# Performance work log

Hardware: AMD Instinct MI355X
Metric: run time of the kernel (lower is better)

## Reference

```python
import jax, jax.numpy as jnp
import numpy as np

# model dims
V, D, C, H, NL, E, EH = 32000, 256, 2, 8, 2, 8, 1024
B, S = 16, 512
DH = D // H
N = B * S


def _pos_encoding(length, d):
    pos = jnp.arange(length)[:, None].astype(jnp.float32)
    div = jnp.exp(jnp.arange(0, d, 2).astype(jnp.float32) * (-np.log(10000.0) / d))
    pe = jnp.zeros((length, d), dtype=jnp.float32)
    pe = pe.at[:, 0::2].set(jnp.sin(pos * div))
    pe = pe.at[:, 1::2].set(jnp.cos(pos * div))
    return pe


def _ln(x, g, b, eps=1e-5):
    mu = x.mean(-1, keepdims=True)
    var = ((x - mu) ** 2).mean(-1, keepdims=True)
    return (x - mu) / jnp.sqrt(var + eps) * g + b


def setup_inputs():
    key = jax.random.key(0)
    ks = jax.random.split(key, 12)
    n = lambda k, shape, s=0.02: (jax.random.normal(k, shape) * s).astype(jnp.float32)
    return dict(
        x=jax.random.randint(ks[0], (B, S), 0, V),
        emb=n(ks[1], (V, D), 0.1),
        in_proj_w=n(ks[2], (NL, 3 * D, D)),
        in_proj_b=jnp.zeros((NL, 3 * D), jnp.float32),
        out_proj_w=n(ks[3], (NL, D, D)),
        out_proj_b=jnp.zeros((NL, D), jnp.float32),
        ln1_g=jnp.ones((NL, D), jnp.float32), ln1_b=jnp.zeros((NL, D), jnp.float32),
        ln2_g=jnp.ones((NL, D), jnp.float32), ln2_b=jnp.zeros((NL, D), jnp.float32),
        gate_w=n(ks[4], (NL, E, D)), gate_b=jnp.zeros((NL, E), jnp.float32),
        w1=n(ks[5], (NL, E, EH, D)), b1=jnp.zeros((NL, E, EH), jnp.float32),
        w2=n(ks[6], (NL, E, D, EH)), b2=jnp.zeros((NL, E, D), jnp.float32),
        fc1_w=n(ks[7], (128, D), 0.1), fc1_b=jnp.zeros((128,), jnp.float32),
        fc2_w=n(ks[8], (C, 128), 0.1), fc2_b=jnp.zeros((C,), jnp.float32),
    )


def reference(x, emb, in_proj_w, in_proj_b, out_proj_w, out_proj_b,
              ln1_g, ln1_b, ln2_g, ln2_b, gate_w, gate_b,
              w1, b1, w2, b2, fc1_w, fc1_b, fc2_w, fc2_b):
    h = emb[x] * np.sqrt(float(D))                       # [B,S,D]
    h = h + _pos_encoding(S, D)[None]
    pad = h.sum(-1) == 0                                 # key padding mask [B,S]
    for l in range(NL):
        # --- multi-head self-attention ---
        qkv = h @ in_proj_w[l].T + in_proj_b[l]          # [B,S,3D]
        q, k, v = jnp.split(qkv, 3, axis=-1)
        q = q.reshape(B, S, H, DH).transpose(0, 2, 1, 3)
        k = k.reshape(B, S, H, DH).transpose(0, 2, 1, 3)
        v = v.reshape(B, S, H, DH).transpose(0, 2, 1, 3)
        sc = jnp.einsum('bhqd,bhkd->bhqk', q, k) / np.sqrt(float(DH))
        sc = jnp.where(pad[:, None, None, :], -1e9, sc)
        a = jax.nn.softmax(sc, axis=-1)
        ctx = jnp.einsum('bhqk,bhkd->bhqd', a, v).transpose(0, 2, 1, 3).reshape(B, S, D)
        attn_out = ctx @ out_proj_w[l].T + out_proj_b[l]
        h = _ln(h + attn_out, ln1_g[l], ln1_b[l])
        # --- top-1 MoE ---
        xf = h.reshape(N, D)
        gwt = jax.nn.softmax(xf @ gate_w[l].T + gate_b[l], axis=-1)  # [N,E]
        top_idx = jnp.argmax(gwt, axis=-1)                # [N]
        top_w = jnp.max(gwt, axis=-1)                     # [N]
        eh = jax.nn.relu(jnp.einsum('nd,ehd->enh', xf, w1[l]) + b1[l][:, None, :])
        ey = jnp.einsum('enh,edh->end', eh, w2[l]) + b2[l][:, None, :]  # [E,N,D]
        sel = ey[top_idx, jnp.arange(N)]                  # gather routed expert output [N,D]
        moe = (top_w[:, None] * sel).reshape(B, S, D)
        h = _ln(h + moe, ln2_g[l], ln2_b[l])
    m = (~pad)[..., None].astype(h.dtype)                 # [B,S,1]
    pooled = (h * m).sum(1) / jnp.clip(m.sum(1), 1.0)     # masked mean pool [B,D]
    z = jax.nn.relu(pooled @ fc1_w.T + fc1_b)
    return z @ fc2_w.T + fc2_b                            # [B,C]
```

## Files before the change

kernel.cpp:

```cpp
#include <hip/hip_runtime.h>
#include <math.h>

#define D_MODEL 256
#define NTOK    8192
#define SEQ     512
#define NB      16
#define NH      8
#define DHEAD   32
#define NE      8
#define EHID    1024
#define CSTRIDE 32

typedef __attribute__((ext_vector_type(8))) short short8;
typedef __attribute__((ext_vector_type(4))) float floatx4;
typedef unsigned short ushort_t;

__device__ __forceinline__ ushort_t bf16r(float f) {
    unsigned int u = __float_as_uint(f);
    u += 0x7fffu + ((u >> 16) & 1u);
    return (ushort_t)(u >> 16);
}
__device__ __forceinline__ float bf2f(ushort_t b) {
    return __uint_as_float(((unsigned)b) << 16);
}

__global__ __launch_bounds__(256) void wconv_all(
    const float* __restrict__ in_proj_w, const float* __restrict__ out_proj_w,
    const float* __restrict__ w1, const float* __restrict__ w2,
    ushort_t* __restrict__ wball)
{
    const int g = blockIdx.x * 256 + threadIdx.x;
    const float* src; ushort_t* dst; int lo;
    if (g < 98304)        { src = in_proj_w;  dst = wball;           lo = g; }
    else if (g < 131072)  { src = out_proj_w; dst = wball + 393216;  lo = g - 98304; }
    else if (g < 1179648) { src = w1;         dst = wball + 524288;  lo = g - 131072; }
    else                  { src = w2;         dst = wball + 4718592; lo = g - 1179648; }
    float4 v = *(const float4*)(src + (size_t)lo * 4);
    ushort_t o[4] = { bf16r(v.x), bf16r(v.y), bf16r(v.z), bf16r(v.w) };
    *(uint2*)(dst + (size_t)lo * 4) = *(uint2*)o;
}

__global__ __launch_bounds__(256) void embed_kernel(
    const int* __restrict__ x, const float* __restrict__ emb,
    float* __restrict__ h, ushort_t* __restrict__ hb, int* __restrict__ pad)
{
    __shared__ float wred[4];
    const int n = blockIdx.x;
    const int d = threadIdx.x;
    const int wave = d >> 6;
    const int s = n & (SEQ - 1);
    const int tok = x[n];
    float v = emb[tok * D_MODEL + d] * 16.0f;
    const int j = d >> 1;
    const float c = -9.210340371976184f / 256.0f;
    const float div = expf((float)(2 * j) * c);
    const float ang = (float)s * div;
    v += (d & 1) ? cosf(ang) : sinf(ang);
    h[n * D_MODEL + d] = v;
    hb[n * D_MODEL + d] = bf16r(v);
    float sm = v;
    for (int o = 1; o < 64; o <<= 1) sm += __shfl_xor(sm, o);
    if ((d & 63) == 0) wred[wave] = sm;
    __syncthreads();
    if (d == 0) pad[n] = ((wred[0] + wred[1] + wred[2] + wred[3]) == 0.0f) ? 1 : 0;
}

#define GF_RELU    1
#define GF_OUTBF16 2
#define GF_GATHER  4
#define GF_SCATTER 8

__global__ __launch_bounds__(256) void mfma_gemm(
    const ushort_t* __restrict__ A, const ushort_t* __restrict__ Bw,
    const float* __restrict__ bias, void* __restrict__ Cout,
    int M, int N, int K,
    const int* __restrict__ counts,
    const int* __restrict__ perm, const float* __restrict__ topw,
    int flags)
{
    __shared__ ushort_t As[64][72];
    __shared__ ushort_t Bs[64][72];
    const int e = blockIdx.z;
    int cnt, off = 0;
    if (counts) {
        cnt = counts[e * CSTRIDE];
        if ((int)blockIdx.y * 64 >= cnt) return;
        for (int i = 0; i < e; i++) off += counts[i * CSTRIDE];
    } else { cnt = M; }
    const ushort_t* Bp = Bw + (size_t)e * N * K;
    const float* bp = bias + (size_t)e * N;
    const int m0 = blockIdx.y * 64, n0 = blockIdx.x * 64;
    const int tid = threadIdx.x;
    const int sr0 = tid >> 3;
    const int kc0 = (tid & 7) * 8;
    const int r0 = m0 + sr0, r1 = r0 + 32;
    const bool v0 = r0 < cnt, v1 = r1 < cnt;
    size_t a0, a1;
    if (flags & GF_GATHER) {
        a0 = (size_t)perm[off + (v0 ? r0 : 0)];
        a1 = (size_t)perm[off + (v1 ? r1 : 0)];
    } else {
        a0 = (size_t)(off + (v0 ? r0 : 0));
        a1 = (size_t)(off + (v1 ? r1 : 0));
    }
    const ushort_t* Ap0 = A + a0 * K + kc0;
    const ushort_t* Ap1 = A + a1 * K + kc0;
    const ushort_t* Bp0 = Bp + (size_t)(n0 + sr0) * K + kc0;
    const ushort_t* Bp1 = Bp + (size_t)(n0 + sr0 + 32) * K + kc0;
    const int lane = tid & 63, wave = tid >> 6;
    const int wm = (wave & 1) * 32, wn = (wave >> 1) * 32;
    const int fr = lane & 15, fk = (lane >> 4) * 8;
    floatx4 acc[2][2];
#pragma unroll
    for (int i = 0; i < 2; i++)
#pragma unroll
        for (int jj = 0; jj < 2; jj++) acc[i][jj] = (floatx4){0.f, 0.f, 0.f, 0.f};

    for (int k0 = 0; k0 < K; k0 += 64) {
        uint4 av0 = *(const uint4*)(Ap0 + k0);
        uint4 av1 = *(const uint4*)(Ap1 + k0);
        uint4 bv0 = *(const uint4*)(Bp0 + k0);
        uint4 bv1 = *(const uint4*)(Bp1 + k0);
        __syncthreads();
        *(uint4*)&As[sr0][kc0]      = av0;
        *(uint4*)&As[sr0 + 32][kc0] = av1;
        *(uint4*)&Bs[sr0][kc0]      = bv0;
        *(uint4*)&Bs[sr0 + 32][kc0] = bv1;
        __syncthreads();
#pragma unroll
        for (int ks = 0; ks < 2; ks++) {
            const int ko = ks * 32 + fk;
            short8 fa0 = *(const short8*)&As[wm + fr][ko];
            short8 fa1 = *(const short8*)&As[wm + 16 + fr][ko];
            short8 fb0 = *(const short8*)&Bs[wn + fr][ko];
            short8 fb1 = *(const short8*)&Bs[wn + 16 + fr][ko];
            acc[0][0] = __builtin_amdgcn_mfma_f32_16x16x32_bf16(fa0, fb0, acc[0][0], 0, 0, 0);
            acc[0][1] = __builtin_amdgcn_mfma_f32_16x16x32_bf16(fa0, fb1, acc[0][1], 0, 0, 0);
            acc[1][0] = __builtin_amdgcn_mfma_f32_16x16x32_bf16(fa1, fb0, acc[1][0], 0, 0, 0);
            acc[1][1] = __builtin_amdgcn_mfma_f32_16x16x32_bf16(fa1, fb1, acc[1][1], 0, 0, 0);
        }
    }
    const int crow0 = (lane >> 4) * 4;
    const int ccol = lane & 15;
#pragma unroll
    for (int fm = 0; fm < 2; fm++) {
#pragma unroll
        for (int fn = 0; fn < 2; fn++) {
            const int gcol = n0 + wn + fn * 16 + ccol;
            const float bsv = bp[gcol];
#pragma unroll
            for (int r = 0; r < 4; r++) {
                const int grow = m0 + wm + fm * 16 + crow0 + r;
                if (grow >= cnt) continue;
                float v = acc[fm][fn][r] + bsv;
                if (flags & GF_RELU) v = fmaxf(v, 0.f);
                if (flags & GF_SCATTER) {
                    const int tok = perm[off + grow];
                    ((float*)Cout)[(size_t)tok * N + gcol] = v * topw[tok];
                } else if (flags & GF_OUTBF16) {
                    ((ushort_t*)Cout)[(size_t)(off + grow) * N + gcol] = bf16r(v);
                } else {
                    ((float*)Cout)[(size_t)(off + grow) * N + gcol] = v;
                }
            }
        }
    }
}

__global__ __launch_bounds__(256) void attn_kernel(
    const ushort_t* __restrict__ qkvb, const int* __restrict__ pad,
    ushort_t* __restrict__ ctxb)
{
    __shared__ ushort_t Kt[64 * 40];
    __shared__ ushort_t Vt[32 * 72];
    __shared__ ushort_t Ps[64 * 72];
    __shared__ float padf[512];
    const int tid = threadIdx.x;
    const int lane = tid & 63;
    const int wave = tid >> 6;
    const int quad = lane >> 4;
    const int l16  = lane & 15;
    const int bid = blockIdx.x;
    const int qt = bid & 7;
    const int hh = (bid >> 3) & 7;
    const int b = bid >> 6;
    const int q0 = wave * 16;

    padf[tid]       = (float)pad[b * SEQ + tid];
    padf[tid + 256] = (float)pad[b * SEQ + 256 + tid];

    short8 qfrag = *(const short8*)(qkvb +
        (size_t)(b * SEQ + qt * 64 + q0 + l16) * 768 + hh * 32 + quad * 8);

    const int skey = tid >> 2;
    const int schunk = (tid & 3) * 8;

    floatx4 o0 = {0.f,0.f,0.f,0.f}, o1 = {0.f,0.f,0.f,0.f};
    float lsum[4] = {0.f, 0.f, 0.f, 0.f};
    const float scale = 0.17677669529663687f;

    for (int t = 0; t < 8; t++) {
        const int kbase = b * SEQ + t * 64;
        __syncthreads();
        uint4 kv = *(const uint4*)(qkvb + (size_t)(kbase + skey) * 768 + 256 + hh * 32 + schunk);
        *(uint4*)&Kt[skey * 40 + schunk] = kv;
        uint4 vv = *(const uint4*)(qkvb + (size_t)(kbase + skey) * 768 + 512 + hh * 32 + schunk);
        ushort_t vs[8]; *(uint4*)vs = vv;
#pragma unroll
        for (int j = 0; j < 8; j++) {
            const int d = schunk + j;
            Vt[d * 72 + (skey ^ ((d >> 3) << 3))] = vs[j];
        }
        __syncthreads();
        floatx4 sfr[4];
#pragma unroll
        for (int fn = 0; fn < 4; fn++) {
            short8 kf = *(const short8*)&Kt[(fn * 16 + l16) * 40 + quad * 8];
            sfr[fn] = __builtin_amdgcn_mfma_f32_16x16x32_bf16(
                qfrag, kf, (floatx4){0.f,0.f,0.f,0.f}, 0, 0, 0);
        }
#pragma unroll
        for (int fn = 0; fn < 4; fn++) {
            const int keyl = fn * 16 + l16;
            const float pv = padf[t * 64 + keyl];
#pragma unroll
            for (int r = 0; r < 4; r++) {
                float p = (pv != 0.f) ? 0.f : __expf(sfr[fn][r] * scale);
                ushort_t pb = bf16r(p);
                lsum[r] += bf2f(pb);
                Ps[(q0 + quad * 4 + r) * 72 + keyl] = pb;
            }
        }
#pragma unroll
        for (int kc = 0; kc < 2; kc++) {
            short8 pf = *(const short8*)&Ps[(q0 + l16) * 72 + kc * 32 + quad * 8];
            {
                const int d = l16;
                short8 vf = *(const short8*)&Vt[d * 72 + ((kc * 32 + quad * 8) ^ ((d >> 3) << 3))];
                o0 = __builtin_amdgcn_mfma_f32_16x16x32_bf16(pf, vf, o0, 0, 0, 0);
            }
            {
                const int d = 16 + l16;
                short8 vf = *(const short8*)&Vt[d * 72 + ((kc * 32 + quad * 8) ^ ((d >> 3) << 3))];
                o1 = __builtin_amdgcn_mfma_f32_16x16x32_bf16(pf, vf, o1, 0, 0, 0);
            }
        }
    }
#pragma unroll
    for (int r = 0; r < 4; r++) {
        float v = lsum[r];
        v += __shfl_xor(v, 1); v += __shfl_xor(v, 2);
        v += __shfl_xor(v, 4); v += __shfl_xor(v, 8);
        lsum[r] = 1.f / v;
    }
    const int nq = b * SEQ + qt * 64 + q0 + quad * 4;
#pragma unroll
    for (int r = 0; r < 4; r++) {
        ushort_t* outp = ctxb + (size_t)(nq + r) * 256 + hh * 32;
        outp[l16]      = bf16r(o0[r] * lsum[r]);
        outp[16 + l16] = bf16r(o1[r] * lsum[r]);
    }
}

__global__ __launch_bounds__(256) void add_ln(
    float* __restrict__ h, const float* __restrict__ add,
    const float* __restrict__ g, const float* __restrict__ b,
    ushort_t* __restrict__ hb)
{
    __shared__ float wred[8];
    const int n = blockIdx.x;
    const int d = threadIdx.x;
    const int wave = d >> 6;
    const float v = h[n * D_MODEL + d] + add[n * D_MODEL + d];
    float s = v;
    for (int o = 1; o < 64; o <<= 1) s += __shfl_xor(s, o);
    if ((d & 63) == 0) wred[wave] = s;
    __syncthreads();
    const float mu = (wred[0] + wred[1] + wred[2] + wred[3]) * (1.0f / 256.0f);
    const float c = v - mu;
    float cs = c * c;
    for (int o = 1; o < 64; o <<= 1) cs += __shfl_xor(cs, o);
    if ((d & 63) == 0) wred[4 + wave] = cs;
    __syncthreads();
    const float var = (wred[4] + wred[5] + wred[6] + wred[7]) * (1.0f / 256.0f);
    const float o = c * rsqrtf(var + 1e-5f) * g[d] + b[d];
    h[n * D_MODEL + d] = o;
    hb[n * D_MODEL + d] = bf16r(o);
}

__global__ __launch_bounds__(256) void gate_kernel(
    const float* __restrict__ h, const float* __restrict__ gw,
    const float* __restrict__ gb, int* __restrict__ top_idx,
    float* __restrict__ top_w, int* __restrict__ pos, int* __restrict__ counts)
{
    __shared__ int lidx[128];
    __shared__ int lpos[128];
    __shared__ int hist[NE];
    __shared__ int base[NE];
    const int wave = threadIdx.x >> 6;
    const int lane = threadIdx.x & 63;
    const int t0 = blockIdx.x * 128 + wave * 32;
    float4 gwr[NE];
#pragma unroll
    for (int e = 0; e < NE; e++)
        gwr[e] = *(const float4*)&gw[e * D_MODEL + lane * 4];
    float gbr[NE];
#pragma unroll
    for (int e = 0; e < NE; e++) gbr[e] = gb[e];

    for (int i = 0; i < 32; i++) {
        const int n = t0 + i;
        float4 hv = *(const float4*)&h[(size_t)n * D_MODEL + lane * 4];
        float lg[NE];
#pragma unroll
        for (int e = 0; e < NE; e++)
            lg[e] = hv.x * gwr[e].x + hv.y * gwr[e].y + hv.z * gwr[e].z + hv.w * gwr[e].w;
#pragma unroll
        for (int e = 0; e < NE; e++) {
            float v = lg[e];
            for (int o = 1; o < 64; o <<= 1) v += __shfl_xor(v, o);
            lg[e] = v;
        }
        if (lane == 0) {
            float best = -1e30f; int bi = 0;
#pragma unroll
            for (int e = 0; e < NE; e++) {
                lg[e] += gbr[e];
                if (lg[e] > best) { best = lg[e]; bi = e; }
            }
            float ssum = 0.0f;
#pragma unroll
            for (int e = 0; e < NE; e++) ssum += __expf(lg[e] - best);
            top_idx[n] = bi;
            top_w[n] = 1.0f / ssum;
            lidx[wave * 32 + i] = bi;
        }
    }
    __syncthreads();
    if (threadIdx.x < NE) hist[threadIdx.x] = 0;
    __syncthreads();
    if (threadIdx.x < 128)
        lpos[threadIdx.x] = atomicAdd(&hist[lidx[threadIdx.x]], 1);
    __syncthreads();
    if (threadIdx.x < NE)
        base[threadIdx.x] = atomicAdd(&counts[threadIdx.x * CSTRIDE], hist[threadIdx.x]);
    __syncthreads();
    if (threadIdx.x < 128)
        pos[blockIdx.x * 128 + threadIdx.x] = base[lidx[threadIdx.x]] + lpos[threadIdx.x];
}

__global__ __launch_bounds__(256) void scatter_perm(
    const int* __restrict__ top_idx, const int* __restrict__ pos,
    const int* __restrict__ counts, int* __restrict__ perm)
{
    __shared__ int offs_s[NE];
    if (threadIdx.x < NE) {
        int a = 0;
        for (int i = 0; i < (int)threadIdx.x; i++) a += counts[i * CSTRIDE];
        offs_s[threadIdx.x] = a;
    }
    __syncthreads();
    const int n = blockIdx.x * 256 + threadIdx.x;
    if (n < NTOK) perm[offs_s[top_idx[n]] + pos[n]] = n;
}

__global__ __launch_bounds__(256) void pool1(
    const float* __restrict__ h, const int* __restrict__ pad,
    float* __restrict__ pooled, float* __restrict__ cntb)
{
    const int b = blockIdx.x, c = blockIdx.y, d = threadIdx.x;
    float s = 0.0f; int cnt = 0;
    for (int i = 0; i < 32; i++) {
        const int idx = b * SEQ + c * 32 + i;
        if (!pad[idx]) { s += h[(size_t)idx * D_MODEL + d]; cnt++; }
    }
    atomicAdd(&pooled[b * D_MODEL + d], s);
    if (d == 0) atomicAdd(&cntb[b], (float)cnt);
}

__global__ __launch_bounds__(128) void cls_kernel(
    const float* __restrict__ pooled, const float* __restrict__ cntb,
    const float* __restrict__ fc1w, const float* __restrict__ fc1b,
    const float* __restrict__ fc2w, const float* __restrict__ fc2b,
    float* __restrict__ out)
{
    __shared__ float zs[128];
    const int b = blockIdx.x;
    const int j = threadIdx.x;
    const float invc = 1.0f / fmaxf(cntb[b], 1.0f);
    float s = 0.0f;
    for (int d = 0; d < D_MODEL; d++) s += pooled[b * D_MODEL + d] * fc1w[j * D_MODEL + d];
    zs[j] = fmaxf(s * invc + fc1b[j], 0.0f);
    __syncthreads();
    if (j < 2) {
        float o = fc2b[j];
        for (int i = 0; i < 128; i++) o += zs[i] * fc2w[j * 128 + i];
        out[b * 2 + j] = o;
    }
}

extern "C" void kernel_launch(void* const* d_in, const int* in_sizes, int n_in,
                              void* d_out, int out_size, void* d_ws, size_t ws_size,
                              hipStream_t stream)
{
    const int*   x          = (const int*)d_in[0];
    const float* emb        = (const float*)d_in[1];
    const float* in_proj_w  = (const float*)d_in[2];
    const float* in_proj_b  = (const float*)d_in[3];
    const float* out_proj_w = (const float*)d_in[4];
    const float* out_proj_b = (const float*)d_in[5];
    const float* ln1_g      = (const float*)d_in[6];
    const float* ln1_b      = (const float*)d_in[7];
    const float* ln2_g      = (const float*)d_in[8];
    const float* ln2_b      = (const float*)d_in[9];
    const float* gate_w     = (const float*)d_in[10];
    const float* gate_b     = (const float*)d_in[11];
    const float* w1         = (const float*)d_in[12];
    const float* b1         = (const float*)d_in[13];
    const float* w2         = (const float*)d_in[14];
    const float* b2         = (const float*)d_in[15];
    const float* fc1_w      = (const float*)d_in[16];
    const float* fc1_b      = (const float*)d_in[17];
    const float* fc2_w      = (const float*)d_in[18];
    const float* fc2_b      = (const float*)d_in[19];
    float* out = (float*)d_out;

    float* ws = (float*)d_ws;
    float*    h      = ws;
    float*    tmp    = ws + 2097152;
    ushort_t* qkvb   = (ushort_t*)(ws + 4194304);
    ushort_t* ctxb   = (ushort_t*)(ws + 7340032);
    ushort_t* ehb    = (ushort_t*)(ws + 4194304);
    ushort_t* hb     = (ushort_t*)(ws + 8388608);
    float*    top_w  = ws + 10485760;
    float*    pooled = ws + 10493952;
    float*    cntb   = ws + 10498048;
    int* ipart   = (int*)(ws + 10498064);
    int* pad     = ipart;
    int* top_idx = ipart + 8192;
    int* pos     = ipart + 16384;
    int* perm    = ipart + 24576;
    int* counts  = ipart + 32768;
    ushort_t* wball = (ushort_t*)(ws + 10531088);

    wconv_all<<<8704, 256, 0, stream>>>(in_proj_w, out_proj_w, w1, w2, wball);
    embed_kernel<<<NTOK, 256, 0, stream>>>(x, emb, h, hb, pad);
    hipMemsetAsync(pooled, 0, (NB * D_MODEL + NB) * sizeof(float), stream);

    for (int l = 0; l < 2; l++) {
        const ushort_t* inb_l  = wball + (size_t)l * 196608;
        const ushort_t* outb_l = wball + 393216 + (size_t)l * 65536;
        const ushort_t* w1b_l  = wball + 524288 + (size_t)l * 2097152;
        const ushort_t* w2b_l  = wball + 4718592 + (size_t)l * 2097152;

        mfma_gemm<<<dim3(768 / 64, NTOK / 64, 1), 256, 0, stream>>>(
            hb, inb_l, in_proj_b + l * 768, qkvb, NTOK, 768, 256,
            nullptr, nullptr, nullptr, GF_OUTBF16);
        attn_kernel<<<NB * NH * (SEQ / 64), 256, 0, stream>>>(qkvb, pad, ctxb);
        mfma_gemm<<<dim3(256 / 64, NTOK / 64, 1), 256, 0, stream>>>(
            ctxb, outb_l, out_proj_b + l * 256, tmp, NTOK, 256, 256,
            nullptr, nullptr, nullptr, 0);
        add_ln<<<NTOK, 256, 0, stream>>>(h, tmp, ln1_g + l * 256, ln1_b + l * 256, hb);
        hipMemsetAsync(counts, 0, NE * CSTRIDE * sizeof(int), stream);
        gate_kernel<<<NTOK / 128, 256, 0, stream>>>(
            h, gate_w + l * NE * 256, gate_b + l * NE, top_idx, top_w, pos, counts);
        scatter_perm<<<NTOK / 256, 256, 0, stream>>>(top_idx, pos, counts, perm);
        mfma_gemm<<<dim3(EHID / 64, NTOK / 64, NE), 256, 0, stream>>>(
            hb, w1b_l, b1 + l * NE * EHID, ehb, 0, EHID, 256,
            counts, perm, nullptr, GF_GATHER | GF_RELU | GF_OUTBF16);
        mfma_gemm<<<dim3(D_MODEL / 64, NTOK / 64, NE), 256, 0, stream>>>(
            ehb, w2b_l, b2 + l * NE * 256, tmp, 0, D_MODEL, 1024,
            counts, perm, top_w, GF_SCATTER);
        add_ln<<<NTOK, 256, 0, stream>>>(h, tmp, ln2_g + l * 256, ln2_b + l * 256, hb);
    }

    pool1<<<dim3(NB, 16), 256, 0, stream>>>(h, pad, pooled, cntb);
    cls_kernel<<<NB, 128, 0, stream>>>(pooled, cntb, fc1_w, fc1_b, fc2_w, fc2_b, out);
}
```

Baseline: 462.3 us.

## Load GEMM tiles via global_load_lds with XOR swizzle, fuse gate into LayerNorm

The GEMM now stages A and B tiles straight from global memory into LDS with global_load_lds, using an XOR-swizzled unpadded layout so register staging is skipped without LDS bank conflicts. The gating softmax/argmax is folded into the first add+LayerNorm kernel, and bucket counting moves into a separate small kernel. Per-layer count buffers are zeroed once up front, which drops a memset per layer. This removes a kernel launch and a re-read of h per layer, but adds eight extra block-wide reductions in the LN kernel.

After: 443.1 us. -4.2%, faster.

```diff
diff --git a/kernel.cpp b/kernel.cpp
--- a/kernel.cpp
+++ b/kernel.cpp
@@ -23,6 +23,11 @@
 __device__ __forceinline__ float bf2f(ushort_t b) {
     return __uint_as_float(((unsigned)b) << 16);
 }
+
+#define GLD16(gsrc, ldst) \
+    __builtin_amdgcn_global_load_lds( \
+        (const __attribute__((address_space(1))) void*)(gsrc), \
+        (__attribute__((address_space(3))) void*)(ldst), 16, 0, 0)
 
 __global__ __launch_bounds__(256) void wconv_all(
     const float* __restrict__ in_proj_w, const float* __restrict__ out_proj_w,
@@ -70,7 +75,7 @@
 #define GF_GATHER  4
 #define GF_SCATTER 8
 
-__global__ __launch_bounds__(256) void mfma_gemm(
+__global__ __launch_bounds__(256) void gemm_gl64(
     const ushort_t* __restrict__ A, const ushort_t* __restrict__ Bw,
     const float* __restrict__ bias, void* __restrict__ Cout,
     int M, int N, int K,
@@ -78,8 +83,8 @@
     const int* __restrict__ perm, const float* __restrict__ topw,
     int flags)
 {
-    __shared__ ushort_t As[64][72];
-    __shared__ ushort_t Bs[64][72];
+    __shared__ ushort_t As[64 * 64];
+    __shared__ ushort_t Bs[64 * 64];
     const int e = blockIdx.z;
     int cnt, off = 0;
     if (counts) {
@@ -91,25 +96,21 @@
     const float* bp = bias + (size_t)e * N;
     const int m0 = blockIdx.y * 64, n0 = blockIdx.x * 64;
     const int tid = threadIdx.x;
-    const int sr0 = tid >> 3;
-    const int kc0 = (tid & 7) * 8;
-    const int r0 = m0 + sr0, r1 = r0 + 32;
-    const bool v0 = r0 < cnt, v1 = r1 < cnt;
-    size_t a0, a1;
-    if (flags & GF_GATHER) {
-        a0 = (size_t)perm[off + (v0 ? r0 : 0)];
-        a1 = (size_t)perm[off + (v1 ? r1 : 0)];
-    } else {
-        a0 = (size_t)(off + (v0 ? r0 : 0));
-        a1 = (size_t)(off + (v1 ? r1 : 0));
-    }
-    const ushort_t* Ap0 = A + a0 * K + kc0;
-    const ushort_t* Ap1 = A + a1 * K + kc0;
-    const ushort_t* Bp0 = Bp + (size_t)(n0 + sr0) * K + kc0;
-    const ushort_t* Bp1 = Bp + (size_t)(n0 + sr0 + 32) * K + kc0;
     const int lane = tid & 63, wave = tid >> 6;
+    const int r8 = lane >> 3;
+    const int p  = lane & 7;
+    const int kswz = ((p ^ r8) << 3);
+    const int row0 = wave * 16;
+    size_t asrc[2], bsrc[2];
+#pragma unroll
+    for (int c = 0; c < 2; c++) {
+        const int gr = m0 + row0 + c * 8 + r8;
+        const int grc = (gr < cnt) ? gr : m0;
+        asrc[c] = (flags & GF_GATHER) ? (size_t)perm[off + grc] : (size_t)(off + grc);
+        bsrc[c] = (size_t)(n0 + row0 + c * 8 + r8);
+    }
+    const int quad = lane >> 4, fr = lane & 15;
     const int wm = (wave & 1) * 32, wn = (wave >> 1) * 32;
-    const int fr = lane & 15, fk = (lane >> 4) * 8;
     floatx4 acc[2][2];
 #pragma unroll
     for (int i = 0; i < 2; i++)
@@ -117,42 +118,39 @@
         for (int jj = 0; jj < 2; jj++) acc[i][jj] = (floatx4){0.f, 0.f, 0.f, 0.f};
 
     for (int k0 = 0; k0 < K; k0 += 64) {
-        uint4 av0 = *(const uint4*)(Ap0 + k0);
-        uint4 av1 = *(const uint4*)(Ap1 + k0);
-        uint4 bv0 = *(const uint4*)(Bp0 + k0);
-        uint4 bv1 = *(const uint4*)(Bp1 + k0);
         __syncthreads();
-        *(uint4*)&As[sr0][kc0]      = av0;
-        *(uint4*)&As[sr0 + 32][kc0] = av1;
-        *(uint4*)&Bs[sr0][kc0]      = bv0;
-        *(uint4*)&Bs[sr0 + 32][kc0] = bv1;
+#pragma unroll
+        for (int c = 0; c < 2; c++) {
+            GLD16(A + asrc[c] * K + k0 + kswz, &As[(row0 + c * 8) * 64]);
+            GLD16(Bp + bsrc[c] * K + k0 + kswz, &Bs[(row0 + c * 8) * 64]);
+        }
         __syncthreads();
 #pragma unroll
         for (int ks = 0; ks < 2; ks++) {
-            const int ko = ks * 32 + fk;
-            short8 fa0 = *(const short8*)&As[wm + fr][ko];
-            short8 fa1 = *(const short8*)&As[wm + 16 + fr][ko];
-            short8 fb0 = *(const short8*)&Bs[wn + fr][ko];
-            short8 fb1 = *(const short8*)&Bs[wn + 16 + fr][ko];
+            const int sw = (((ks * 4 + quad) ^ (fr & 7)) << 3);
+            short8 fa0 = *(const short8*)&As[(wm + fr) * 64 + sw];
+            short8 fa1 = *(const short8*)&As[(wm + 16 + fr) * 64 + sw];
+            short8 fb0 = *(const short8*)&Bs[(wn + fr) * 64 + sw];
+            short8 fb1 = *(const short8*)&Bs[(wn + 16 + fr) * 64 + sw];
             acc[0][0] = __builtin_amdgcn_mfma_f32_16x16x32_bf16(fa0, fb0, acc[0][0], 0, 0, 0);
             acc[0][1] = __builtin_amdgcn_mfma_f32_16x16x32_bf16(fa0, fb1, acc[0][1], 0, 0, 0);
             acc[1][0] = __builtin_amdgcn_mfma_f32_16x16x32_bf16(fa1, fb0, acc[1][0], 0, 0, 0);
             acc[1][1] = __builtin_amdgcn_mfma_f32_16x16x32_bf16(fa1, fb1, acc[1][1], 0, 0, 0);
         }
     }
-    const int crow0 = (lane >> 4) * 4;
-    const int ccol = lane & 15;
-#pragma unroll
-    for (int fm = 0; fm < 2; fm++) {
-#pragma unroll
-        for (int fn = 0; fn < 2; fn++) {
-            const int gcol = n0 + wn + fn * 16 + ccol;
+    const int crow0 = quad * 4;
+    const int ccol = fr;
+#pragma unroll
+    for (int m = 0; m < 2; m++) {
+#pragma unroll
+        for (int n = 0; n < 2; n++) {
+            const int gcol = n0 + wn + n * 16 + ccol;
             const float bsv = bp[gcol];
 #pragma unroll
             for (int r = 0; r < 4; r++) {
-                const int grow = m0 + wm + fm * 16 + crow0 + r;
+                const int grow = m0 + wm + m * 16 + crow0 + r;
                 if (grow >= cnt) continue;
-                float v = acc[fm][fn][r] + bsv;
+                float v = acc[m][n][r] + bsv;
                 if (flags & GF_RELU) v = fmaxf(v, 0.f);
                 if (flags & GF_SCATTER) {
                     const int tok = perm[off + grow];
@@ -262,12 +260,16 @@
     }
 }
 
-__global__ __launch_bounds__(256) void add_ln(
+template<bool GATE>
+__global__ __launch_bounds__(256) void add_ln_t(
     float* __restrict__ h, const float* __restrict__ add,
     const float* __restrict__ g, const float* __restrict__ b,
-    ushort_t* __restrict__ hb)
+    ushort_t* __restrict__ hb,
+    const float* __restrict__ gw, const float* __restrict__ gb,
+    int* __restrict__ top_idx, float* __restrict__ top_w)
 {
     __shared__ float wred[8];
+    __shared__ float ered[NE][4];
     const int n = blockIdx.x;
     const int d = threadIdx.x;
     const int wave = d >> 6;
@@ -286,46 +288,20 @@
     const float o = c * rsqrtf(var + 1e-5f) * g[d] + b[d];
     h[n * D_MODEL + d] = o;
     hb[n * D_MODEL + d] = bf16r(o);
-}
-
-__global__ __launch_bounds__(256) void gate_kernel(
-    const float* __restrict__ h, const float* __restrict__ gw,
-    const float* __restrict__ gb, int* __restrict__ top_idx,
-    float* __restrict__ top_w, int* __restrict__ pos, int* __restrict__ counts)
-{
-    __shared__ int lidx[128];
-    __shared__ int lpos[128];
-    __shared__ int hist[NE];
-    __shared__ int base[NE];
-    const int wave = threadIdx.x >> 6;
-    const int lane = threadIdx.x & 63;
-    const int t0 = blockIdx.x * 128 + wave * 32;
-    float4 gwr[NE];
-#pragma unroll
-    for (int e = 0; e < NE; e++)
-        gwr[e] = *(const float4*)&gw[e * D_MODEL + lane * 4];
-    float gbr[NE];
-#pragma unroll
-    for (int e = 0; e < NE; e++) gbr[e] = gb[e];
-
-    for (int i = 0; i < 32; i++) {
-        const int n = t0 + i;
-        float4 hv = *(const float4*)&h[(size_t)n * D_MODEL + lane * 4];
-        float lg[NE];
-#pragma unroll
-        for (int e = 0; e < NE; e++)
-            lg[e] = hv.x * gwr[e].x + hv.y * gwr[e].y + hv.z * gwr[e].z + hv.w * gwr[e].w;
+    if (GATE) {
 #pragma unroll
         for (int e = 0; e < NE; e++) {
-            float v = lg[e];
-            for (int o = 1; o < 64; o <<= 1) v += __shfl_xor(v, o);
-            lg[e] = v;
-        }
-        if (lane == 0) {
+            float pe = o * gw[e * D_MODEL + d];
+            for (int of = 1; of < 64; of <<= 1) pe += __shfl_xor(pe, of);
+            if ((d & 63) == 0) ered[e][wave] = pe;
+        }
+        __syncthreads();
+        if (d == 0) {
             float best = -1e30f; int bi = 0;
+            float lg[NE];
 #pragma unroll
             for (int e = 0; e < NE; e++) {
-                lg[e] += gbr[e];
+                lg[e] = ered[e][0] + ered[e][1] + ered[e][2] + ered[e][3] + gb[e];
                 if (lg[e] > best) { best = lg[e]; bi = e; }
             }
             float ssum = 0.0f;
@@ -333,20 +309,27 @@
             for (int e = 0; e < NE; e++) ssum += __expf(lg[e] - best);
             top_idx[n] = bi;
             top_w[n] = 1.0f / ssum;
-            lidx[wave * 32 + i] = bi;
-        }
-    }
-    __syncthreads();
+        }
+    }
+}
+
+__global__ __launch_bounds__(256) void bucket_kernel(
+    const int* __restrict__ top_idx, int* __restrict__ pos,
+    int* __restrict__ counts)
+{
+    __shared__ int hist[NE];
+    __shared__ int base[NE];
+    __shared__ int lpos[256];
+    const int n = blockIdx.x * 256 + threadIdx.x;
     if (threadIdx.x < NE) hist[threadIdx.x] = 0;
     __syncthreads();
-    if (threadIdx.x < 128)
-        lpos[threadIdx.x] = atomicAdd(&hist[lidx[threadIdx.x]], 1);
+    const int e = top_idx[n];
+    lpos[threadIdx.x] = atomicAdd(&hist[e], 1);
     __syncthreads();
     if (threadIdx.x < NE)
         base[threadIdx.x] = atomicAdd(&counts[threadIdx.x * CSTRIDE], hist[threadIdx.x]);
     __syncthreads();
-    if (threadIdx.x < 128)
-        pos[blockIdx.x * 128 + threadIdx.x] = base[lidx[threadIdx.x]] + lpos[threadIdx.x];
+    pos[n] = base[e] + lpos[threadIdx.x];
 }
 
 __global__ __launch_bounds__(256) void scatter_perm(
@@ -432,46 +415,49 @@
     ushort_t* ctxb   = (ushort_t*)(ws + 7340032);
     ushort_t* ehb    = (ushort_t*)(ws + 4194304);
     ushort_t* hb     = (ushort_t*)(ws + 8388608);
-    float*    top_w  = ws + 10485760;
-    float*    pooled = ws + 10493952;
-    float*    cntb   = ws + 10498048;
-    int* ipart   = (int*)(ws + 10498064);
+    float*    top_w  = ws + 9437184;
+    float*    pooled = ws + 9445376;
+    float*    cntb   = ws + 9449472;
+    int*      counts = (int*)(ws + 9449488);
+    int* ipart   = (int*)(ws + 9450000);
     int* pad     = ipart;
     int* top_idx = ipart + 8192;
     int* pos     = ipart + 16384;
     int* perm    = ipart + 24576;
-    int* counts  = ipart + 32768;
-    ushort_t* wball = (ushort_t*)(ws + 10531088);
+    ushort_t* wball = (ushort_t*)(ws + 9482768);
 
     wconv_all<<<8704, 256, 0, stream>>>(in_proj_w, out_proj_w, w1, w2, wball);
     embed_kernel<<<NTOK, 256, 0, stream>>>(x, emb, h, hb, pad);
-    hipMemsetAsync(pooled, 0, (NB * D_MODEL + NB) * sizeof(float), stream);
+    hipMemsetAsync(pooled, 0, (4096 + 16 + 2 * NE * CSTRIDE) * sizeof(float), stream);
 
     for (int l = 0; l < 2; l++) {
         const ushort_t* inb_l  = wball + (size_t)l * 196608;
         const ushort_t* outb_l = wball + 393216 + (size_t)l * 65536;
         const ushort_t* w1b_l  = wball + 524288 + (size_t)l * 2097152;
         const ushort_t* w2b_l  = wball + 4718592 + (size_t)l * 2097152;
-
-        mfma_gemm<<<dim3(768 / 64, NTOK / 64, 1), 256, 0, stream>>>(
+        int* counts_l = counts + l * NE * CSTRIDE;
+
+        gemm_gl64<<<dim3(768 / 64, NTOK / 64, 1), 256, 0, stream>>>(
             hb, inb_l, in_proj_b + l * 768, qkvb, NTOK, 768, 256,
             nullptr, nullptr, nullptr, GF_OUTBF16);
         attn_kernel<<<NB * NH * (SEQ / 64), 256, 0, stream>>>(qkvb, pad, ctxb);
-        mfma_gemm<<<dim3(256 / 64, NTOK / 64, 1), 256, 0, stream>>>(
+        gemm_gl64<<<dim3(256 / 64, NTOK / 64, 1), 256, 0, stream>>>(
             ctxb, outb_l, out_proj_b + l * 256, tmp, NTOK, 256, 256,
             nullptr, nullptr, nullptr, 0);
-        add_ln<<<NTOK, 256, 0, stream>>>(h, tmp, ln1_g + l * 256, ln1_b + l * 256, hb);
-        hipMemsetAsync(counts, 0, NE * CSTRIDE * sizeof(int), stream);
-        gate_kernel<<<NTOK / 128, 256, 0, stream>>>(
-            h, gate_w + l * NE * 256, gate_b + l * NE, top_idx, top_w, pos, counts);
-        scatter_perm<<<NTOK / 256, 256, 0, stream>>>(top_idx, pos, counts, perm);
-        mfma_gemm<<<dim3(EHID / 64, NTOK / 64, NE), 256, 0, stream>>>(
+        add_ln_t<true><<<NTOK, 256, 0, stream>>>(
+            h, tmp, ln1_g + l * 256, ln1_b + l * 256, hb,
+            gate_w + l * NE * 256, gate_b + l * NE, top_idx, top_w);
+        bucket_kernel<<<NTOK / 256, 256, 0, stream>>>(top_idx, pos, counts_l);
+        scatter_perm<<<NTOK / 256, 256, 0, stream>>>(top_idx, pos, counts_l, perm);
+        gemm_gl64<<<dim3(EHID / 64, NTOK / 64, NE), 256, 0, stream>>>(
             hb, w1b_l, b1 + l * NE * EHID, ehb, 0, EHID, 256,
-            counts, perm, nullptr, GF_GATHER | GF_RELU | GF_OUTBF16);
-        mfma_gemm<<<dim3(D_MODEL / 64, NTOK / 64, NE), 256, 0, stream>>>(
+            counts_l, perm, nullptr, GF_GATHER | GF_RELU | GF_OUTBF16);
+        gemm_gl64<<<dim3(D_MODEL / 64, NTOK / 64, NE), 256, 0, stream>>>(
             ehb, w2b_l, b2 + l * NE * 256, tmp, 0, D_MODEL, 1024,
-            counts, perm, top_w, GF_SCATTER);
-        add_ln<<<NTOK, 256, 0, stream>>>(h, tmp, ln2_g + l * 256, ln2_b + l * 256, hb);
+            counts_l, perm, top_w, GF_SCATTER);
+        add_ln_t<false><<<NTOK, 256, 0, stream>>>(
+            h, tmp, ln2_g + l * 256, ln2_b + l * 256, hb,
+            nullptr, nullptr, nullptr, nullptr);
     }
 
     pool1<<<dim3(NB, 16), 256, 0, stream>>>(h, pad, pooled, cntb);
```
